# Kernel optimization log

Measured on AMD Instinct MI355X. Metric: run time of the kernel, lower is better.

## Reference

```python
import jax, jax.numpy as jnp
import numpy as np

B, N, NPOINT = 8, 131072, 1024


def setup_inputs() -> dict:
    key = jax.random.key(0)
    in1 = jax.random.normal(key, (B, N, 3), dtype=jnp.float32)
    return {"in1": in1, "out1": NPOINT}


def _fps_indices(xyz, npoint):
    # xyz: [B, N, 3] -> indices [B, npoint] via iterative farthest point sampling.
    b, n, _ = xyz.shape
    init_mindist = jnp.full((b, n), jnp.inf, dtype=xyz.dtype)
    init_farthest = jnp.zeros((b,), dtype=jnp.int32)  # start from point 0

    def step(carry, _):
        mindist, farthest = carry
        # centroid: [B, 1, 3] -- the most recently selected point per batch
        centroid = jnp.take_along_axis(xyz, farthest[:, None, None], axis=1)
        d = jnp.sum((xyz - centroid) ** 2, axis=-1)  # [B, N] squared distances
        mindist = jnp.minimum(mindist, d)
        nxt = jnp.argmax(mindist, axis=-1).astype(jnp.int32)  # farthest remaining point
        return (mindist, nxt), farthest

    (_, _), idx = jax.lax.scan(step, (init_mindist, init_farthest), None, length=npoint)
    return idx.T  # [B, npoint]


def reference(in1, out1):
    # Faithful FPS semantics of custom_ops.test_fps: sample out1 farthest points.
    idx = _fps_indices(in1, out1)                        # [B, npoint]
    sampled = jnp.take_along_axis(in1, idx[:, :, None], axis=1)  # [B, npoint, 3]
    return sampled
```

## Files before the change

### kernel.cpp

```cpp
#include <hip/hip_runtime.h>
#include <cstdint>


constexpr int kB = 8;
constexpr int kN = 131072;
constexpr int kNpoint = 1024;
constexpr int kBlocksPerBatch = 16;
constexpr int kThreads = 1024;
constexpr int kPPT = 8;
constexpr int kPtsPerBlock = kThreads * kPPT;

__device__ __forceinline__ uint64_t u64max(uint64_t a, uint64_t b) {
    return a > b ? a : b;
}

__device__ __forceinline__ uint64_t shfl_xor_u64(uint64_t v, int m) {
    int lo = __shfl_xor((int)(uint32_t)v, m, 64);
    int hi = __shfl_xor((int)(uint32_t)(v >> 32), m, 64);
    return ((uint64_t)(uint32_t)hi << 32) | (uint32_t)lo;
}

__global__ __launch_bounds__(kThreads, 4) void fps_kernel(
        const float* __restrict__ xyz, float* __restrict__ out,
        uint64_t* __restrict__ slots) {
    const int b    = blockIdx.x & 7;
    const int blk  = blockIdx.x >> 3;
    const int tid  = threadIdx.x;
    const int lane = tid & 63;
    const int wid  = tid >> 6;

    const float* __restrict__ base = xyz + (size_t)b * kN * 3;

    float x[kPPT], y[kPPT], z[kPPT], md[kPPT];
#pragma unroll
    for (int j = 0; j < kPPT; ++j) {
        const int p = blk * kPtsPerBlock + j * kThreads + tid;
        x[j] = base[3 * p + 0];
        y[j] = base[3 * p + 1];
        z[j] = base[3 * p + 2];
        md[j] = __builtin_inff();
    }

    float cx = base[0], cy = base[1], cz = base[2];
    if (blk == 0 && tid == 0) {
        float* o = out + (size_t)b * kNpoint * 3;
        o[0] = cx; o[1] = cy; o[2] = cz;
    }

    __shared__ uint64_t warr[kThreads / 64];
    __shared__ float cent[3];

    for (int t = 1; t < kNpoint; ++t) {
        uint64_t best = 0;
#pragma unroll
        for (int j = 0; j < kPPT; ++j) {
            const float dx = __fsub_rn(x[j], cx);
            const float dy = __fsub_rn(y[j], cy);
            const float dz = __fsub_rn(z[j], cz);
            const float d  = __fadd_rn(__fadd_rn(__fmul_rn(dx, dx), __fmul_rn(dy, dy)),
                                       __fmul_rn(dz, dz));
            const float m = fminf(md[j], d);
            md[j] = m;
            const uint32_t p = (uint32_t)(blk * kPtsPerBlock + j * kThreads + tid);
            const uint64_t pk = ((uint64_t)__float_as_uint(m) << 17) | ((~p) & 0x1FFFFu);
            best = u64max(best, pk);
        }

#pragma unroll
        for (int s = 32; s > 0; s >>= 1) best = u64max(best, shfl_xor_u64(best, s));
        if (lane == 0) warr[wid] = best;
        __syncthreads();

        if (wid == 0) {
            uint64_t* slotbuf = slots + ((size_t)(t & 1) * kB + b) * kBlocksPerBatch;

            uint64_t v = (lane < kThreads / 64) ? warr[lane] : 0;
#pragma unroll
            for (int s = 8; s > 0; s >>= 1) v = u64max(v, shfl_xor_u64(v, s));

            if (lane == 0) {
                __hip_atomic_store(&slotbuf[blk], ((uint64_t)t << 49) | v,
                                   __ATOMIC_RELAXED, __HIP_MEMORY_SCOPE_AGENT);
            }

            uint64_t got = 0;
            bool need = lane < kBlocksPerBatch;
            while (__any(need)) {
                if (need) {
                    uint64_t sv = __hip_atomic_load(&slotbuf[lane], __ATOMIC_RELAXED,
                                                    __HIP_MEMORY_SCOPE_AGENT);
                    if ((sv >> 49) == (uint64_t)t) { got = sv; need = false; }
                }
            }
#pragma unroll
            for (int s = 8; s > 0; s >>= 1) got = u64max(got, shfl_xor_u64(got, s));

            if (lane == 0) {
                const uint32_t widx = 131071u - (uint32_t)(got & 0x1FFFFu);
                const float wx = base[3 * (size_t)widx + 0];
                const float wy = base[3 * (size_t)widx + 1];
                const float wz = base[3 * (size_t)widx + 2];
                cent[0] = wx; cent[1] = wy; cent[2] = wz;
                if (blk == 0) {
                    float* o = out + ((size_t)b * kNpoint + t) * 3;
                    o[0] = wx; o[1] = wy; o[2] = wz;
                }
            }
        }
        __syncthreads();
        cx = cent[0]; cy = cent[1]; cz = cent[2];
    }
}

extern "C" void kernel_launch(void* const* d_in, const int* in_sizes, int n_in,
                              void* d_out, int out_size, void* d_ws, size_t ws_size,
                              hipStream_t stream) {
    const float* xyz = (const float*)d_in[0];
    float* out = (float*)d_out;
    uint64_t* slots = (uint64_t*)d_ws;
    fps_kernel<<<dim3(kB * kBlocksPerBatch), dim3(kThreads), 0, stream>>>(xyz, out, slots);
}
```

Before: 2.365 ms.

## Replace shuffle reductions with DPP, LDS atomic max, and per-wave global polling

Wave reductions now use DPP row operations instead of ds_bpermute shuffles, and the block reduction uses an LDS atomic max into a double-buffered slot, which drops one __syncthreads per iteration. Every wave now polls the 16 global slots itself and loads the new centroid directly, so the LDS broadcast and second barrier go away. The per-thread argmax is done as a float compare before packing, avoiding a 64-bit max per point. The cost is heavier polling traffic on global memory from all 16 waves per block, and a possible race on the lbest slot's reset between iterations.

```diff
diff --git a/kernel.cpp b/kernel.cpp
--- a/kernel.cpp
+++ b/kernel.cpp
@@ -14,10 +14,29 @@
     return a > b ? a : b;
 }
 
-__device__ __forceinline__ uint64_t shfl_xor_u64(uint64_t v, int m) {
-    int lo = __shfl_xor((int)(uint32_t)v, m, 64);
-    int hi = __shfl_xor((int)(uint32_t)(v >> 32), m, 64);
+template <int CTRL>
+__device__ __forceinline__ uint64_t dpp_u64(uint64_t v) {
+    int lo = __builtin_amdgcn_update_dpp(0, (int)(uint32_t)v, CTRL, 0xF, 0xF, false);
+    int hi = __builtin_amdgcn_update_dpp(0, (int)(uint32_t)(v >> 32), CTRL, 0xF, 0xF, false);
     return ((uint64_t)(uint32_t)hi << 32) | (uint32_t)lo;
+}
+
+__device__ __forceinline__ uint64_t wave_max_to_lane63(uint64_t v) {
+    v = u64max(v, dpp_u64<0x111>(v));
+    v = u64max(v, dpp_u64<0x112>(v));
+    v = u64max(v, dpp_u64<0x114>(v));
+    v = u64max(v, dpp_u64<0x118>(v));
+    v = u64max(v, dpp_u64<0x142>(v));
+    v = u64max(v, dpp_u64<0x143>(v));
+    return v;
+}
+
+__device__ __forceinline__ uint64_t group16_max(uint64_t v) {
+    v = u64max(v, dpp_u64<0xB1>(v));
+    v = u64max(v, dpp_u64<0x4E>(v));
+    v = u64max(v, dpp_u64<0x141>(v));
+    v = u64max(v, dpp_u64<0x140>(v));
+    return v;
 }
 
 __global__ __launch_bounds__(kThreads, 4) void fps_kernel(
@@ -27,7 +46,6 @@
     const int blk  = blockIdx.x >> 3;
     const int tid  = threadIdx.x;
     const int lane = tid & 63;
-    const int wid  = tid >> 6;
 
     const float* __restrict__ base = xyz + (size_t)b * kN * 3;
 
@@ -41,17 +59,19 @@
         md[j] = __builtin_inff();
     }
 
+    __shared__ uint64_t lbest[2];
+    if (tid == 0) { lbest[0] = 0; lbest[1] = 0; }
+
     float cx = base[0], cy = base[1], cz = base[2];
     if (blk == 0 && tid == 0) {
         float* o = out + (size_t)b * kNpoint * 3;
         o[0] = cx; o[1] = cy; o[2] = cz;
     }
-
-    __shared__ uint64_t warr[kThreads / 64];
-    __shared__ float cent[3];
+    __syncthreads();
 
     for (int t = 1; t < kNpoint; ++t) {
-        uint64_t best = 0;
+        float bm = -1.0f;
+        int bj = 0;
 #pragma unroll
         for (int j = 0; j < kPPT; ++j) {
             const float dx = __fsub_rn(x[j], cx);
@@ -61,54 +81,48 @@
                                        __fmul_rn(dz, dz));
             const float m = fminf(md[j], d);
             md[j] = m;
-            const uint32_t p = (uint32_t)(blk * kPtsPerBlock + j * kThreads + tid);
-            const uint64_t pk = ((uint64_t)__float_as_uint(m) << 17) | ((~p) & 0x1FFFFu);
-            best = u64max(best, pk);
+            const bool g = m > bm;
+            bj = g ? j : bj;
+            bm = g ? m : bm;
+        }
+        const uint32_t p = (uint32_t)(blk * kPtsPerBlock + bj * kThreads + tid);
+        uint64_t pk = ((uint64_t)t << 49) |
+                      ((uint64_t)__float_as_uint(bm) << 17) |
+                      ((~p) & 0x1FFFFu);
+
+        pk = wave_max_to_lane63(pk);
+        if (lane == 63) {
+            __hip_atomic_fetch_max(&lbest[t & 1], pk, __ATOMIC_RELAXED,
+                                   __HIP_MEMORY_SCOPE_WORKGROUP);
+        }
+        __syncthreads();
+
+        uint64_t* slotbuf = slots + ((size_t)(t & 1) * kB + b) * kBlocksPerBatch;
+        if (tid == 0) {
+            __hip_atomic_store(&slotbuf[blk], lbest[t & 1], __ATOMIC_RELAXED,
+                               __HIP_MEMORY_SCOPE_AGENT);
         }
 
-#pragma unroll
-        for (int s = 32; s > 0; s >>= 1) best = u64max(best, shfl_xor_u64(best, s));
-        if (lane == 0) warr[wid] = best;
-        __syncthreads();
-
-        if (wid == 0) {
-            uint64_t* slotbuf = slots + ((size_t)(t & 1) * kB + b) * kBlocksPerBatch;
-
-            uint64_t v = (lane < kThreads / 64) ? warr[lane] : 0;
-#pragma unroll
-            for (int s = 8; s > 0; s >>= 1) v = u64max(v, shfl_xor_u64(v, s));
-
-            if (lane == 0) {
-                __hip_atomic_store(&slotbuf[blk], ((uint64_t)t << 49) | v,
-                                   __ATOMIC_RELAXED, __HIP_MEMORY_SCOPE_AGENT);
-            }
-
-            uint64_t got = 0;
-            bool need = lane < kBlocksPerBatch;
-            while (__any(need)) {
-                if (need) {
-                    uint64_t sv = __hip_atomic_load(&slotbuf[lane], __ATOMIC_RELAXED,
-                                                    __HIP_MEMORY_SCOPE_AGENT);
-                    if ((sv >> 49) == (uint64_t)t) { got = sv; need = false; }
-                }
-            }
-#pragma unroll
-            for (int s = 8; s > 0; s >>= 1) got = u64max(got, shfl_xor_u64(got, s));
-
-            if (lane == 0) {
-                const uint32_t widx = 131071u - (uint32_t)(got & 0x1FFFFu);
-                const float wx = base[3 * (size_t)widx + 0];
-                const float wy = base[3 * (size_t)widx + 1];
-                const float wz = base[3 * (size_t)widx + 2];
-                cent[0] = wx; cent[1] = wy; cent[2] = wz;
-                if (blk == 0) {
-                    float* o = out + ((size_t)b * kNpoint + t) * 3;
-                    o[0] = wx; o[1] = wy; o[2] = wz;
-                }
+        uint64_t got = 0;
+        bool need = lane < kBlocksPerBatch;
+        while (__any(need)) {
+            if (need) {
+                uint64_t sv = __hip_atomic_load(&slotbuf[lane], __ATOMIC_RELAXED,
+                                                __HIP_MEMORY_SCOPE_AGENT);
+                if ((sv >> 49) == (uint64_t)t) { got = sv; need = false; }
             }
         }
-        __syncthreads();
-        cx = cent[0]; cy = cent[1]; cz = cent[2];
+        got = group16_max(got);
+
+        const uint32_t lo = (uint32_t)got;
+        const uint32_t widx = 131071u - (__builtin_amdgcn_readfirstlane((int)lo) & 0x1FFFFu);
+        cx = base[3 * (size_t)widx + 0];
+        cy = base[3 * (size_t)widx + 1];
+        cz = base[3 * (size_t)widx + 2];
+        if (blk == 0 && tid == 0) {
+            float* o = out + ((size_t)b * kNpoint + t) * 3;
+            o[0] = cx; o[1] = cy; o[2] = cz;
+        }
     }
 }
 
```

Result: faster. 2.027 ms (-14.3%).
